# Kernel tuning notes

Measured on AMD Instinct MI355X. Metric: run time of the kernel, lower is better.

## Reference

```python
import jax, jax.numpy as jnp
import numpy as np

KS = 3           # kernel size (conv1, conv2, deform conv)
PAD = 1          # k//2 padding for the dense convs and deform zero-padding
DIM = 256
B, H, W = 4, 64, 64
N = KS * KS      # number of sampling points per output pixel


def conv2d(x, w, b=None, pad=PAD, stride=1):
    out = jax.lax.conv_general_dilated(
        x, w, (stride, stride), [(pad, pad), (pad, pad)],
        dimension_numbers=('NCHW', 'OIHW', 'NCHW'))
    if b is not None:
        out = out + b[None, :, None, None]
    return out


def deform_conv(x, p_w, p_b, dw):
    # DeformConv2d (deform-conv-v2 style, modulation=False)
    b, c, h, w = x.shape
    offset = conv2d(x, p_w, p_b, pad=1)                     # (b, 2N, h, w)
    xp = jnp.pad(x, ((0, 0), (0, 0), (PAD, PAD), (PAD, PAD)))
    Hp, Wp = h + 2 * PAD, w + 2 * PAD

    # kernel-relative offsets p_n: rows first, then cols (row-major flatten)
    r = jnp.arange(-(KS - 1) // 2, (KS - 1) // 2 + 1, dtype=x.dtype)
    pnx, pny = jnp.meshgrid(r, r, indexing='ij')
    p_n = jnp.concatenate([pnx.ravel(), pny.ravel()])       # (2N,)

    # base grid p_0 starts at 1 (consistent with zero padding of 1)
    gy, gx = jnp.meshgrid(jnp.arange(1, h + 1, dtype=x.dtype),
                          jnp.arange(1, w + 1, dtype=x.dtype), indexing='ij')
    p0 = jnp.concatenate([jnp.tile(gy[..., None], (1, 1, N)),
                          jnp.tile(gx[..., None], (1, 1, N))], axis=-1)  # (h,w,2N)

    p = jnp.transpose(offset, (0, 2, 3, 1)) + p_n + p0      # (b,h,w,2N)
    px, py = p[..., :N], p[..., N:]
    fx, fy = jnp.floor(px), jnp.floor(py)
    qlx = jnp.clip(fx, 0, Hp - 1)
    qly = jnp.clip(fy, 0, Wp - 1)
    qrx = jnp.clip(fx + 1, 0, Hp - 1)
    qry = jnp.clip(fy + 1, 0, Wp - 1)
    px = jnp.clip(px, 0, Hp - 1)
    py = jnp.clip(py, 0, Wp - 1)

    # bilinear weights
    g_lt = (1 + qlx - px) * (1 + qly - py)
    g_rb = (1 - qrx + px) * (1 - qry + py)
    g_lb = (1 + qlx - px) * (1 - qry + py)
    g_rt = (1 - qrx + px) * (1 + qly - py)

    xf = xp.reshape(b, c, Hp * Wp)

    def gather(qx, qy):
        idx = (qx.astype(jnp.int32) * Wp + qy.astype(jnp.int32)).reshape(b, -1)
        return jax.vmap(lambda xb, ib: xb[:, ib])(xf, idx).reshape(b, c, h, w, N)

    x_off = (g_lt[:, None] * gather(qlx, qly) + g_rb[:, None] * gather(qrx, qry)
           + g_lb[:, None] * gather(qlx, qry) + g_rt[:, None] * gather(qrx, qly))

    # (b,c,h,w,N) -> (b,c,h*ks,w*ks): kernel row expands h, kernel col expands w
    x_off = x_off.reshape(b, c, h, w, KS, KS).transpose(0, 1, 2, 4, 3, 5)
    x_off = x_off.reshape(b, c, h * KS, w * KS)
    return conv2d(x_off, dw, None, pad=0, stride=KS)       # (b, c, h, w)


def setup_inputs() -> dict:
    key = jax.random.key(0)
    ks = jax.random.split(key, 8)
    s = 1.0 / np.sqrt(DIM * KS * KS)
    return {
        'x':   jax.random.normal(ks[0], (B, DIM, H, W), jnp.float32),
        'w1':  jax.random.normal(ks[1], (DIM, DIM, KS, KS), jnp.float32) * s,
        'b1':  jax.random.normal(ks[2], (DIM,), jnp.float32) * 0.01,
        'w2':  jax.random.normal(ks[3], (DIM, DIM, KS, KS), jnp.float32) * s,
        'b2':  jax.random.normal(ks[4], (DIM,), jnp.float32) * 0.01,
        'p_w': jax.random.normal(ks[5], (2 * N, DIM, 3, 3), jnp.float32) * (0.05 * s),
        'p_b': jnp.zeros((2 * N,), jnp.float32),
        'dw':  jax.random.normal(ks[6], (DIM, DIM, KS, KS), jnp.float32) * s,
    }


def reference(x, w1, b1, w2, b2, p_w, p_b, dw):
    res = jax.nn.relu(conv2d(x, w1, b1, pad=PAD))   # conv1 + ReLU
    res = res + x                                   # residual 1
    res = conv2d(res, w2, b2, pad=PAD)              # conv2
    res = deform_conv(res, p_w, p_b, dw)            # deformable conv
    return res + x                                  # residual 2
```

## Files before the change

kernel.cpp:

```cpp
#include <hip/hip_runtime.h>

#define HW 64
#define NB 4
#define CH 256

typedef __attribute__((address_space(1))) const void* gptr_t;
typedef __attribute__((address_space(3))) void* lptr_t;
typedef __attribute__((ext_vector_type(8))) short bf8v;
typedef __attribute__((ext_vector_type(4))) float f32x4;

__device__ __forceinline__ void gll16(const void* g, void* l) {
  __builtin_amdgcn_global_load_lds((gptr_t)g, (lptr_t)l, 16, 0, 0);
}
__device__ __forceinline__ ushort f2b(float f) {
  union { float f; uint u; } v; v.f = f;
  uint r = v.u + 0x7FFF + ((v.u >> 16) & 1);
  return (ushort)(r >> 16);
}
__device__ __forceinline__ uint cvt_pk_bf16(float lo, float hi) {
  uint r;
  asm("v_cvt_pk_bf16_f32 %0, %1, %2" : "=v"(r) : "v"(lo), "v"(hi));
  return r;
}
__device__ __forceinline__ float asf(uint u) {
  union { uint u; float f; } v; v.u = u; return v.f;
}

__device__ __forceinline__ void combine_store(
    const uint4& c0, const uint4& c1, const uint4& c2, const uint4& c3,
    const float4& gw, ushort* dst)
{
  uint o[4];
  const uint* p0 = (const uint*)&c0; const uint* p1 = (const uint*)&c1;
  const uint* p2 = (const uint*)&c2; const uint* p3 = (const uint*)&c3;
  #pragma unroll
  for (int w = 0; w < 4; ++w) {
    const float lo = gw.x * asf(p0[w] << 16) + gw.y * asf(p1[w] << 16)
                   + gw.z * asf(p2[w] << 16) + gw.w * asf(p3[w] << 16);
    const float hi = gw.x * asf(p0[w] & 0xffff0000u) + gw.y * asf(p1[w] & 0xffff0000u)
                   + gw.z * asf(p2[w] & 0xffff0000u) + gw.w * asf(p3[w] & 0xffff0000u);
    o[w] = cvt_pk_bf16(lo, hi);
  }
  uint4 r; r.x = o[0]; r.y = o[1]; r.z = o[2]; r.w = o[3];
  *(uint4*)dst = r;
}

__global__ __launch_bounds__(256) void zero_borders_k(
    ushort* __restrict__ xpad, ushort* __restrict__ res1, ushort* __restrict__ res2)
{
  const int buf = blockIdx.x >> 2, b = blockIdx.x & 3;
  ushort* base = (buf == 0 ? xpad : buf == 1 ? res1 : res2) + (size_t)b * 4356 * 256;
  uint4 z; z.x = 0; z.y = 0; z.z = 0; z.w = 0;
  for (int u = threadIdx.x; u < 260 * 32; u += 256) {
    const int p = u >> 5, k = u & 31;
    int r, cc;
    if (p < 66)       { r = 0;       cc = p; }
    else if (p < 132) { r = 65;      cc = p - 66; }
    else if (p < 196) { r = p - 131; cc = 0; }
    else              { r = p - 195; cc = 65; }
    *(uint4*)&base[((size_t)r * 66 + cc) * 256 + k * 8] = z;
  }
}

__global__ __launch_bounds__(256) void pack_x_k(
    const float* __restrict__ x, ushort* __restrict__ xpad)
{
  __shared__ float tile[64][261];
  const int t = threadIdx.x, b = blockIdx.x >> 6, i = blockIdx.x & 63;
  const int wave = t >> 6, l = t & 63;
  const float* src = x + (size_t)b * CH * 4096 + (size_t)i * 64;
  for (int cc = 0; cc < 64; ++cc) {
    const int c = cc * 4 + wave;
    tile[l][c] = src[(size_t)c * 4096 + l];
  }
  __syncthreads();
  const int c0 = (t & 31) * 8;
  #pragma unroll
  for (int jj = 0; jj < 8; ++jj) {
    const int j = (t >> 5) + jj * 8;
    const float4 v0 = *(const float4*)&tile[j][c0];
    const float4 v1 = *(const float4*)&tile[j][c0 + 4];
    uint4 o;
    o.x = cvt_pk_bf16(v0.x, v0.y);
    o.y = cvt_pk_bf16(v0.z, v0.w);
    o.z = cvt_pk_bf16(v1.x, v1.y);
    o.w = cvt_pk_bf16(v1.z, v1.w);
    *(uint4*)&xpad[((size_t)b * 4356 + (i + 1) * 66 + (j + 1)) * 256 + c0] = o;
  }
}

__global__ __launch_bounds__(256) void pack_w_k(
    const float* __restrict__ w1, const float* __restrict__ w2,
    const float* __restrict__ dw, const float* __restrict__ pw,
    const float* __restrict__ pb,
    ushort* __restrict__ wpk1, ushort* __restrict__ wpk2,
    ushort* __restrict__ dwpk, ushort* __restrict__ wpkO, float* __restrict__ pbias)
{
  const int id = blockIdx.x * 256 + threadIdx.x;
  if (id < 3 * 73728) {
    const int tsel = id / 73728, r = id % 73728;
    const int kc = r & 3, o = (r >> 2) & 255, ct = r >> 10;
    const int cb = ct / 9, tap = ct % 9;
    const float* w = (tsel == 0) ? w1 : (tsel == 1) ? w2 : dw;
    const float* s = w + ((size_t)o * CH + cb * 32 + kc * 8) * 9 + tap;
    ushort* d = ((tsel == 0) ? wpk1 : (tsel == 1) ? wpk2 : dwpk) + (size_t)r * 8;
    #pragma unroll
    for (int j = 0; j < 8; ++j) d[j] = f2b(s[j * 9]);
  } else if (id < 3 * 73728 + 9216) {
    const int r = id - 3 * 73728;
    const int kc = r & 3, o = (r >> 2) & 31, ct = r >> 7;
    const int cb = ct / 9, tap = ct % 9;
    ushort* d = wpkO + (size_t)r * 8;
    if (o < 18) {
      const float* s = pw + ((size_t)o * CH + cb * 32 + kc * 8) * 9 + tap;
      #pragma unroll
      for (int j = 0; j < 8; ++j) d[j] = f2b(s[j * 9]);
    } else {
      #pragma unroll
      for (int j = 0; j < 8; ++j) d[j] = 0;
    }
  }
  if (id < 32) pbias[id] = (id < 18) ? pb[id] : 0.f;
}

template<int OTOT, int OUTMODE>
__global__ __launch_bounds__(256, 2) void conv_mfma(
    const ushort* __restrict__ apad, const ushort* __restrict__ wpk,
    const float* __restrict__ bias, const float* __restrict__ xres,
    void* __restrict__ outp)
{
  __shared__ __align__(16) ushort patch[2][6336];
  const int t = threadIdx.x, wave = t >> 6, l = t & 63;
  const int ot  = (OTOT == 256) ? (blockIdx.x >> 8) : 0;
  const int rem = blockIdx.x & 255;
  const int b = rem >> 6, i = rem & 63;
  const int ln = l & 15, kc8 = (l >> 4) * 8;

  constexpr int FO = 2;
  constexpr int FP = (OTOT == 256) ? 4 : 1;
  const int oS  = (OTOT == 256) ? (ot * 128 + wave * 32) : 0;
  const int pxB = (OTOT == 256) ? 0 : (wave * 16);

  const ushort* rowbase = apad + ((size_t)(b * 66 + i) * 66) * 256;

  f32x4 acc[FO][FP];
  #pragma unroll
  for (int a = 0; a < FO; ++a)
    #pragma unroll
    for (int d = 0; d < FP; ++d) acc[a][d] = (f32x4){0.f, 0.f, 0.f, 0.f};

  #define STAGE(buf, cb)                                                        \
    _Pragma("unroll")                                                           \
    for (int it = 0; it < 4; ++it) {                                            \
      const int e = t + it * 256;                                               \
      if (it < 3 || t < 24) {                                                   \
        const int r = e / 264, u = e - r * 264;                                 \
        const int p = r * 66 + (u >> 2);                                        \
        const int sl = (u & 3) ^ ((p >> 1) & 3);                                \
        const ushort* s = rowbase + (size_t)p * 256 + (cb) * 32 + sl * 8;       \
        gll16(s, (ushort*)&patch[buf][0] + (size_t)e * 8);                      \
      }                                                                         \
    }

  STAGE(0, 0)
  for (int cb = 0; cb < 8; ++cb) {
    __syncthreads();
    const ushort* pbuf = &patch[cb & 1][0];
    #pragma unroll
    for (int ch = 0; ch < 3; ++ch) {
      bf8v wfr[3][FO];
      #pragma unroll
      for (int q = 0; q < 3; ++q) {
        const int tap = ch * 3 + q;
        #pragma unroll
        for (int fo = 0; fo < FO; ++fo)
          wfr[q][fo] = *(const bf8v*)&wpk[((size_t)((cb * 9 + tap) * OTOT) + oS + fo * 16 + ln) * 32 + kc8];
      }
      if (ch == 2 && cb < 7) { STAGE((cb + 1) & 1, cb + 1) }
      __builtin_amdgcn_s_setprio(1);
      #pragma unroll
      for (int q = 0; q < 3; ++q) {
        const int tap = ch * 3 + q;
        const int ky = tap / 3, kx = tap % 3;
        #pragma unroll
        for (int fp = 0; fp < FP; ++fp) {
          const int px = pxB + fp * 16 + ln;
          const int pix = ky * 66 + px + kx;
          const int sl = (l >> 4) ^ ((pix >> 1) & 3);
          const bf8v pf = *(const bf8v*)&pbuf[pix * 32 + sl * 8];
          #pragma unroll
          for (int fo = 0; fo < FO; ++fo)
            acc[fo][fp] = __builtin_amdgcn_mfma_f32_16x16x32_bf16(wfr[q][fo], pf, acc[fo][fp], 0, 0, 0);
        }
      }
      __builtin_amdgcn_s_setprio(0);
    }
  }
  #undef STAGE

  #pragma unroll
  for (int fo = 0; fo < FO; ++fo) {
    #pragma unroll
    for (int fp = 0; fp < FP; ++fp) {
      const f32x4 a = acc[fo][fp];
      const int o = oS + fo * 16 + (l >> 4) * 4;
      const int j = pxB + fp * 16 + ln;
      const float4 bv = *(const float4*)&bias[o];
      float v0 = a[0] + bv.x, v1 = a[1] + bv.y, v2 = a[2] + bv.z, v3 = a[3] + bv.w;
      if (OUTMODE == 0) {
        const size_t xb = (((size_t)b * CH + o) * HW + i) * HW + j;
        v0 = fmaxf(v0, 0.f) + xres[xb];
        v1 = fmaxf(v1, 0.f) + xres[xb + 4096];
        v2 = fmaxf(v2, 0.f) + xres[xb + 8192];
        v3 = fmaxf(v3, 0.f) + xres[xb + 12288];
      }
      if (OUTMODE == 2) {
        float* op = (float*)outp + ((size_t)b * 4096 + i * 64 + j) * 32 + o;
        float4 r; r.x = v0; r.y = v1; r.z = v2; r.w = v3;
        *(float4*)op = r;
      } else {
        ushort* op = (ushort*)outp + ((size_t)b * 4356 + (i + 1) * 66 + (j + 1)) * 256 + o;
        ushort4 s; s.x = f2b(v0); s.y = f2b(v1); s.z = f2b(v2); s.w = f2b(v3);
        *(ushort4*)op = s;
      }
    }
  }
}

__global__ __launch_bounds__(512, 2) void deform_mfma(
    const ushort* __restrict__ res2pad, const float* __restrict__ offs,
    const ushort* __restrict__ dwpk, const float* __restrict__ x,
    float* __restrict__ out)
{
  __shared__ __align__(16) ushort samp[2][18432];
  __shared__ __align__(16) int    tblI[576 * 4];
  __shared__ __align__(16) float  tblW[576 * 4];

  const int t = threadIdx.x, wave = t >> 6, l = t & 63;
  const int blk = (blockIdx.x & 7) * 32 + (blockIdx.x >> 3);
  const int b = blk >> 6, i = blk & 63;
  const int ln = l & 15, kc8 = (l >> 4) * 8;
  const int oS = wave * 32;

  #pragma unroll
  for (int k2 = 0; k2 < 2; ++k2) {
    const int e = t + k2 * 512;
    if (e < 576) {
      const int n = e >> 6, j = e & 63;
      const int ki = n / 3, kj = n % 3;
      const float offr = offs[((size_t)(b * 64 + i) * 64 + j) * 32 + n];
      const float offc = offs[((size_t)(b * 64 + i) * 64 + j) * 32 + 9 + n];
      const float prow = offr + (float)(ki - 1) + (float)(i + 1);
      const float pcol = offc + (float)(kj - 1) + (float)(j + 1);
      const float fx = floorf(prow), fy = floorf(pcol);
      const float qlx = fminf(fmaxf(fx, 0.f), 65.f);
      const float qly = fminf(fmaxf(fy, 0.f), 65.f);
      const float qrx = fminf(fmaxf(fx + 1.f, 0.f), 65.f);
      const float qry = fminf(fmaxf(fy + 1.f, 0.f), 65.f);
      const float pr  = fminf(fmaxf(prow, 0.f), 65.f);
      const float pc  = fminf(fmaxf(pcol, 0.f), 65.f);
      tblI[e * 4 + 0] = ((int)qlx * 66 + (int)qly) * 512;
      tblI[e * 4 + 1] = ((int)qrx * 66 + (int)qry) * 512;
      tblI[e * 4 + 2] = ((int)qlx * 66 + (int)qry) * 512;
      tblI[e * 4 + 3] = ((int)qrx * 66 + (int)qly) * 512;
      tblW[e * 4 + 0] = (1.f + qlx - pr) * (1.f + qly - pc);
      tblW[e * 4 + 1] = (1.f - qrx + pr) * (1.f - qry + pc);
      tblW[e * 4 + 2] = (1.f + qlx - pr) * (1.f - qry + pc);
      tblW[e * 4 + 3] = (1.f - qrx + pr) * (1.f + qly - pc);
    }
  }

  f32x4 acc[2][4];
  #pragma unroll
  for (int a = 0; a < 2; ++a)
    #pragma unroll
    for (int d = 0; d < 4; ++d) acc[a][d] = (f32x4){0.f, 0.f, 0.f, 0.f};

  const char* res2b = (const char*)(res2pad + (size_t)b * 4356 * 256);

  #define SAMPLE_CB(cb_, buf_)                                                  \
    _Pragma("unroll")                                                           \
    for (int k = 0; k < 5; ++k) {                                               \
      if (k < 4 || t < 256) {                                                   \
        const int u = t + k * 512;                                              \
        const int e = u >> 2, i16 = u & 3;                                      \
        const int4 iv = *(const int4*)&tblI[e * 4];                             \
        const float4 gw = *(const float4*)&tblW[e * 4];                         \
        const char* gb = res2b + (cb_) * 64 + i16 * 16;                         \
        const uint4 c0 = *(const uint4*)(gb + iv.x);                            \
        const uint4 c1 = *(const uint4*)(gb + iv.y);                            \
        const uint4 c2 = *(const uint4*)(gb + iv.z);                            \
        const uint4 c3 = *(const uint4*)(gb + iv.w);                            \
        const int sl = i16 ^ ((e >> 1) & 3);                                    \
        combine_store(c0, c1, c2, c3, gw, &samp[buf_][(size_t)e * 32 + sl * 8]);\
      }                                                                         \
    }

  __syncthreads();
  SAMPLE_CB(0, 0)
  __syncthreads();

  const int rsl = ((l >> 4) ^ ((ln >> 1) & 3)) * 8;

  for (int cb = 0; cb < 8; ++cb) {
    const ushort* sb = &samp[cb & 1][0];
    const ushort* wbase = dwpk + (size_t)(cb * 9) * 256 * 32;

    #pragma unroll
    for (int ch = 0; ch < 3; ++ch) {
      bf8v bfr[3][2];
      #pragma unroll
      for (int q = 0; q < 3; ++q)
        #pragma unroll
        for (int fo = 0; fo < 2; ++fo)
          bfr[q][fo] = *(const bf8v*)&wbase[((size_t)((ch * 3 + q) * 256) + oS + fo * 16 + ln) * 32 + kc8];
      __builtin_amdgcn_s_setprio(1);
      #pragma unroll
      for (int q = 0; q < 3; ++q) {
        const int tap = ch * 3 + q;
        #pragma unroll
        for (int fp = 0; fp < 4; ++fp) {
          const bf8v af = *(const bf8v*)&sb[(tap * 64 + fp * 16 + ln) * 32 + rsl];
          #pragma unroll
          for (int fo = 0; fo < 2; ++fo)
            acc[fo][fp] = __builtin_amdgcn_mfma_f32_16x16x32_bf16(af, bfr[q][fo], acc[fo][fp], 0, 0, 0);
        }
      }
      __builtin_amdgcn_s_setprio(0);
    }

    if (cb < 7) { SAMPLE_CB(cb + 1, (cb + 1) & 1) }
    __syncthreads();
  }
  #undef SAMPLE_CB

  #pragma unroll
  for (int fo = 0; fo < 2; ++fo) {
    #pragma unroll
    for (int fp = 0; fp < 4; ++fp) {
      const f32x4 a = acc[fo][fp];
      const int o = oS + fo * 16 + ln;
      const int j0 = fp * 16 + (l >> 4) * 4;
      const size_t base = (((size_t)b * CH + o) * HW + i) * HW + j0;
      const float4 xv = *(const float4*)&x[base];
      float4 r; r.x = a[0] + xv.x; r.y = a[1] + xv.y; r.z = a[2] + xv.z; r.w = a[3] + xv.w;
      *(float4*)&out[base] = r;
    }
  }
}

extern "C" void kernel_launch(void* const* d_in, const int* in_sizes, int n_in,
                              void* d_out, int out_size, void* d_ws, size_t ws_size,
                              hipStream_t stream) {
  (void)in_sizes; (void)n_in; (void)out_size; (void)ws_size;
  const float* x  = (const float*)d_in[0];
  const float* w1 = (const float*)d_in[1];
  const float* b1 = (const float*)d_in[2];
  const float* w2 = (const float*)d_in[3];
  const float* b2 = (const float*)d_in[4];
  const float* pw = (const float*)d_in[5];
  const float* pb = (const float*)d_in[6];
  const float* dw = (const float*)d_in[7];
  float* out = (float*)d_out;

  char* w = (char*)d_ws;
  size_t off = 0;
  auto carve = [&](size_t bytes) { char* p = w + off; off += (bytes + 255) & ~(size_t)255; return p; };
  ushort* xpad  = (ushort*)carve(8929280);
  ushort* res1  = (ushort*)carve(8929280);
  ushort* res2  = (ushort*)carve(8929280);
  ushort* wpk1  = (ushort*)carve(1179648);
  ushort* wpk2  = (ushort*)carve(1179648);
  ushort* wpkO  = (ushort*)carve(147456);
  ushort* dwpk  = (ushort*)carve(1179648);
  float*  pbias = (float*) carve(256);
  float*  offs  = (float*) carve(2097152);

  zero_borders_k<<<12, 256, 0, stream>>>(xpad, res1, res2);
  pack_w_k<<<900, 256, 0, stream>>>(w1, w2, dw, pw, pb, wpk1, wpk2, dwpk, wpkO, pbias);
  pack_x_k<<<256, 256, 0, stream>>>(x, xpad);
  conv_mfma<256, 0><<<512, 256, 0, stream>>>(xpad, wpk1, b1, x, res1);
  conv_mfma<256, 1><<<512, 256, 0, stream>>>(res1, wpk2, b2, nullptr, res2);
  conv_mfma<32, 2><<<256, 256, 0, stream>>>(res2, wpkO, pbias, nullptr, offs);
  deform_mfma<<<NB * HW, 512, 0, stream>>>(res2, offs, dwpk, x, out);
}
```

Baseline: 129.3 us.

## Hoist gather tables to registers and software-pipeline gathers and weight loads

```diff
diff --git a/kernel.cpp b/kernel.cpp
--- a/kernel.cpp
+++ b/kernel.cpp
@@ -269,6 +269,22 @@
       tblW[e * 4 + 3] = (1.f - qrx + pr) * (1.f + qly - pc);
     }
   }
+  __syncthreads();
+
+  int4   ivr[5];
+  float4 gwr[5];
+  #pragma unroll
+  for (int k = 0; k < 5; ++k) {
+    if (k < 4 || t < 256) {
+      const int u = (k < 4) ? (t + k * 512) : (2048 + t);
+      const int e = u >> 2;
+      int4 iv = *(const int4*)&tblI[e * 4];
+      const int fold = (t & 3) * 16;
+      iv.x += fold; iv.y += fold; iv.z += fold; iv.w += fold;
+      ivr[k] = iv;
+      gwr[k] = *(const float4*)&tblW[e * 4];
+    }
+  }
 
   f32x4 acc[2][4];
   #pragma unroll
@@ -277,62 +293,83 @@
     for (int d = 0; d < 4; ++d) acc[a][d] = (f32x4){0.f, 0.f, 0.f, 0.f};
 
   const char* res2b = (const char*)(res2pad + (size_t)b * 4356 * 256);
-
-  #define SAMPLE_CB(cb_, buf_)                                                  \
+  const int rsl = ((l >> 4) ^ ((ln >> 1) & 3)) * 8;
+
+  #define GATH(gp, k_, cb_) {                                                   \
+      const char* gbp_ = res2b + (cb_) * 64;                                    \
+      gp##0 = *(const uint4*)(gbp_ + ivr[k_].x);                                \
+      gp##1 = *(const uint4*)(gbp_ + ivr[k_].y);                                \
+      gp##2 = *(const uint4*)(gbp_ + ivr[k_].z);                                \
+      gp##3 = *(const uint4*)(gbp_ + ivr[k_].w);                                \
+    }
+  #define COMB(gp, k_, buf_) {                                                  \
+      const int e_ = ((k_) < 4) ? ((t + (k_) * 512) >> 2) : ((2048 + t) >> 2);  \
+      const int sl_ = (t & 3) ^ ((e_ >> 1) & 3);                                \
+      combine_store(gp##0, gp##1, gp##2, gp##3, gwr[k_],                        \
+                    &samp[buf_][(size_t)e_ * 32 + sl_ * 8]);                    \
+    }
+  #define SAMPLE_PIPE(cb_, buf_) {                                              \
+      uint4 gA0, gA1, gA2, gA3, gB0, gB1, gB2, gB3;                             \
+      GATH(gA, 0, cb_)                                                          \
+      GATH(gB, 1, cb_)                                                          \
+      COMB(gA, 0, buf_)                                                         \
+      GATH(gA, 2, cb_)                                                          \
+      COMB(gB, 1, buf_)                                                         \
+      GATH(gB, 3, cb_)                                                          \
+      COMB(gA, 2, buf_)                                                         \
+      if (t < 256) { GATH(gA, 4, cb_) }                                         \
+      COMB(gB, 3, buf_)                                                         \
+      if (t < 256) { COMB(gA, 4, buf_) }                                        \
+    }
+  #define LOADW(dst, cb_, ch_)                                                  \
     _Pragma("unroll")                                                           \
-    for (int k = 0; k < 5; ++k) {                                               \
-      if (k < 4 || t < 256) {                                                   \
-        const int u = t + k * 512;                                              \
-        const int e = u >> 2, i16 = u & 3;                                      \
-        const int4 iv = *(const int4*)&tblI[e * 4];                             \
-        const float4 gw = *(const float4*)&tblW[e * 4];                         \
-        const char* gb = res2b + (cb_) * 64 + i16 * 16;                         \
-        const uint4 c0 = *(const uint4*)(gb + iv.x);                            \
-        const uint4 c1 = *(const uint4*)(gb + iv.y);                            \
-        const uint4 c2 = *(const uint4*)(gb + iv.z);                            \
-        const uint4 c3 = *(const uint4*)(gb + iv.w);                            \
-        const int sl = i16 ^ ((e >> 1) & 3);                                    \
-        combine_store(c0, c1, c2, c3, gw, &samp[buf_][(size_t)e * 32 + sl * 8]);\
+    for (int q = 0; q < 3; ++q) {                                               \
+      _Pragma("unroll")                                                         \
+      for (int fo = 0; fo < 2; ++fo)                                            \
+        dst[q][fo] = *(const bf8v*)&dwpk[((size_t)(((cb_) * 9 + (ch_) * 3 + q) * 256) + oS + fo * 16 + ln) * 32 + kc8]; \
+    }
+  #define MFMACH(ch_, wset) {                                                   \
+      __builtin_amdgcn_s_setprio(1);                                            \
+      _Pragma("unroll")                                                         \
+      for (int q = 0; q < 3; ++q) {                                             \
+        const int tap_ = (ch_) * 3 + q;                                         \
+        _Pragma("unroll")                                                       \
+        for (int fp = 0; fp < 4; ++fp) {                                        \
+          const bf8v af_ = *(const bf8v*)&sb[(tap_ * 64 + fp * 16 + ln) * 32 + rsl]; \
+          _Pragma("unroll")                                                     \
+          for (int fo = 0; fo < 2; ++fo)                                        \
+            acc[fo][fp] = __builtin_amdgcn_mfma_f32_16x16x32_bf16(af_, wset[q][fo], acc[fo][fp], 0, 0, 0); \
+        }                                                                       \
       }                                                                         \
-    }
-
+      __builtin_amdgcn_s_setprio(0);                                            \
+    }
+  #define BODY(cb_, WC, WN) {                                                   \
+      const ushort* sb = &samp[(cb_) & 1][0];                                   \
+      LOADW(WN, cb_, 1)                                                         \
+      MFMACH(0, WC)                                                             \
+      LOADW(WC, cb_, 2)                                                         \
+      MFMACH(1, WN)                                                             \
+      if ((cb_) < 7) { LOADW(WN, (cb_) + 1, 0) }                                \
+      MFMACH(2, WC)                                                             \
+      if ((cb_) < 7) { SAMPLE_PIPE((cb_) + 1, ((cb_) + 1) & 1) }                \
+      __syncthreads();                                                          \
+    }
+
+  bf8v wA[3][2], wB[3][2];
+  LOADW(wA, 0, 0)
+  SAMPLE_PIPE(0, 0)
   __syncthreads();
-  SAMPLE_CB(0, 0)
-  __syncthreads();
-
-  const int rsl = ((l >> 4) ^ ((ln >> 1) & 3)) * 8;
-
-  for (int cb = 0; cb < 8; ++cb) {
-    const ushort* sb = &samp[cb & 1][0];
-    const ushort* wbase = dwpk + (size_t)(cb * 9) * 256 * 32;
-
-    #pragma unroll
-    for (int ch = 0; ch < 3; ++ch) {
-      bf8v bfr[3][2];
-      #pragma unroll
-      for (int q = 0; q < 3; ++q)
-        #pragma unroll
-        for (int fo = 0; fo < 2; ++fo)
-          bfr[q][fo] = *(const bf8v*)&wbase[((size_t)((ch * 3 + q) * 256) + oS + fo * 16 + ln) * 32 + kc8];
-      __builtin_amdgcn_s_setprio(1);
-      #pragma unroll
-      for (int q = 0; q < 3; ++q) {
-        const int tap = ch * 3 + q;
-        #pragma unroll
-        for (int fp = 0; fp < 4; ++fp) {
-          const bf8v af = *(const bf8v*)&sb[(tap * 64 + fp * 16 + ln) * 32 + rsl];
-          #pragma unroll
-          for (int fo = 0; fo < 2; ++fo)
-            acc[fo][fp] = __builtin_amdgcn_mfma_f32_16x16x32_bf16(af, bfr[q][fo], acc[fo][fp], 0, 0, 0);
-        }
-      }
-      __builtin_amdgcn_s_setprio(0);
-    }
-
-    if (cb < 7) { SAMPLE_CB(cb + 1, (cb + 1) & 1) }
-    __syncthreads();
-  }
-  #undef SAMPLE_CB
+
+  for (int h = 0; h < 4; ++h) {
+    BODY(2 * h, wA, wB)
+    BODY(2 * h + 1, wB, wA)
+  }
+  #undef BODY
+  #undef MFMACH
+  #undef LOADW
+  #undef SAMPLE_PIPE
+  #undef COMB
+  #undef GATH
 
   #pragma unroll
   for (int fo = 0; fo < 2; ++fo) {
```

New measurement: 131.9 us. +2.1%, slower.
